# Kernel tuning notes

Hardware: AMD Instinct MI355X
Metric: run time of the kernel (lower is better)

The kernel has to match this reference:

```python
import jax, jax.numpy as jnp
import numpy as np

B, H, S, D = 2, 16, 2048, 128


def setup_inputs() -> dict:
    key = jax.random.key(0)
    kq, kk, kv, km, kb = jax.random.split(key, 5)
    q = jax.random.normal(kq, (B, H, S, D), dtype=jnp.float32)
    k = jax.random.normal(kk, (B, H, S, D), dtype=jnp.float32)
    v = jax.random.normal(kv, (B, H, S, D), dtype=jnp.float32)
    mask = jax.random.randint(km, (B, 1, S, S), 0, 2, dtype=jnp.int32)
    rel_bias = jax.random.normal(kb, (H, S, S), dtype=jnp.float32)
    return {"q": q, "k": k, "v": v, "mask": mask, "rel_bias": rel_bias}


def reference(q, k, v, mask, rel_bias):
    d_k = q.shape[-1]
    scale = 1.0 / jnp.sqrt(jnp.float32(d_k)).astype(q.dtype)
    # scores: [B,H,S,S]
    scores = jnp.einsum("bhqd,bhkd->bhqk", q, k) * scale
    scores = scores + rel_bias[None, :, :, :]  # broadcast batch
    NEG = jnp.asarray(-1e9, dtype=scores.dtype)
    scores = jnp.where(mask == 0, NEG, scores)
    attn = jax.nn.softmax(scores, axis=-1)
    # dropout p=0.0 -> identity (reference uses eval/deterministic dropout)
    out = jnp.einsum("bhqk,bhkd->bhqd", attn, v)
    return (out, attn)
```

## Files before the change

### kernel.cpp

```cpp
#include <hip/hip_runtime.h>

#define B_ 2
#define H_ 16
#define S_ 2048
#define D_ 128

typedef __attribute__((ext_vector_type(8))) short short8;
typedef __attribute__((ext_vector_type(4))) float floatx4;

__device__ __forceinline__ unsigned short f2bf(float f) {
    union { float f; unsigned int u; } c; c.f = f;
    unsigned int u = c.u;
    u += 0x7fff + ((u >> 16) & 1);
    return (unsigned short)(u >> 16);
}

__global__ __launch_bounds__(256) void vt_kernel(const float* __restrict__ v,
                                                 unsigned short* __restrict__ vt) {
    __shared__ unsigned short tl[128][66];
    int bid = blockIdx.x;
    int bh = bid >> 5;
    int s0 = (bid & 31) << 6;
    int t = threadIdx.x;
    const float4* vp = (const float4*)(v + ((size_t)bh * S_ + s0) * D_);
    #pragma unroll
    for (int i = 0; i < 8; ++i) {
        int idx = t + i * 256;
        int r = idx >> 5;
        int d = (idx & 31) << 2;
        float4 x = vp[idx];
        tl[d + 0][r] = f2bf(x.x);
        tl[d + 1][r] = f2bf(x.y);
        tl[d + 2][r] = f2bf(x.z);
        tl[d + 3][r] = f2bf(x.w);
    }
    __syncthreads();
    unsigned short* op = vt + (size_t)bh * D_ * S_ + s0;
    #pragma unroll
    for (int i = 0; i < 16; ++i) {
        int idx = t + i * 256;
        int d = idx >> 5;
        int s2 = (idx & 31) << 1;
        unsigned int val = (unsigned int)tl[d][s2] | ((unsigned int)tl[d][s2 + 1] << 16);
        *(unsigned int*)(op + (size_t)d * S_ + s2) = val;
    }
}

__global__ __launch_bounds__(256, 4) void qk_kernel(const float* __restrict__ q,
                                                    const float* __restrict__ k,
                                                    const int* __restrict__ mask,
                                                    const float* __restrict__ bias,
                                                    float* __restrict__ attn,
                                                    float* __restrict__ lsum) {
    __shared__ unsigned short q_lds[64 * 136];
    __shared__ __align__(16) char ks[17408];
    unsigned short* k_lds = (unsigned short*)ks;
    float* s_lds = (float*)ks;

    int bid = blockIdx.x;
    int qt = bid >> 5;
    int hb = bid & 31;
    int h = hb >> 1;
    int b = hb & 1;
    int bh = b * H_ + h;
    int q0 = qt << 6;
    int t = threadIdx.x;
    int w = t >> 6;
    int lane = t & 63;
    int g = lane >> 4;
    int l16 = lane & 15;
    int tr = t >> 4;
    int tc = (t & 15) << 2;

    const float4* qp = (const float4*)(q + ((size_t)bh * S_ + q0) * D_);
    #pragma unroll
    for (int i = 0; i < 8; ++i) {
        int idx = t + i * 256;
        int r = idx >> 5;
        int d = (idx & 31) << 2;
        float4 x = qp[idx];
        ushort4 y;
        y.x = f2bf(x.x); y.y = f2bf(x.y); y.z = f2bf(x.z); y.w = f2bf(x.w);
        *(ushort4*)&q_lds[r * 136 + d] = y;
    }
    __syncthreads();

    short8 afr[4];
    {
        int ro = (w * 16 + l16) * 136 + g * 8;
        #pragma unroll
        for (int kk = 0; kk < 4; ++kk)
            afr[kk] = *(const short8*)&q_lds[ro + kk * 32];
    }

    const float scale = 0.08838834764831845f;
    float rs[4] = {0.f, 0.f, 0.f, 0.f};
    const float* bias_h = bias + (size_t)h * S_ * S_;
    const int* mask_b = mask + (size_t)b * S_ * S_;
    float* attn_p = attn + (size_t)bh * S_ * S_;
    const float4* kbase = (const float4*)(k + (size_t)bh * S_ * D_);

    for (int kt = 0; kt < 32; ++kt) {
        int k0 = kt << 6;
        __syncthreads();
        const float4* kp = kbase + (size_t)k0 * (D_ / 4);
        float4 kv[8];
        #pragma unroll
        for (int i = 0; i < 8; ++i) kv[i] = kp[t + i * 256];
        float4 b4[4];
        int4 m4[4];
        #pragma unroll
        for (int i = 0; i < 4; ++i) {
            size_t off = (size_t)(q0 + tr + 16 * i) * S_ + k0 + tc;
            b4[i] = *(const float4*)&bias_h[off];
            m4[i] = *(const int4*)&mask_b[off];
        }
        #pragma unroll
        for (int i = 0; i < 8; ++i) {
            int idx = t + i * 256;
            int r = idx >> 5;
            int d = (idx & 31) << 2;
            ushort4 y;
            y.x = f2bf(kv[i].x); y.y = f2bf(kv[i].y); y.z = f2bf(kv[i].z); y.w = f2bf(kv[i].w);
            *(ushort4*)&k_lds[r * 136 + d] = y;
        }
        __syncthreads();

        floatx4 acc[4];
        #pragma unroll
        for (int nt = 0; nt < 4; ++nt) acc[nt] = (floatx4){0.f, 0.f, 0.f, 0.f};
        #pragma unroll
        for (int kk = 0; kk < 4; ++kk) {
            #pragma unroll
            for (int nt = 0; nt < 4; ++nt) {
                short8 bfr = *(const short8*)&k_lds[(nt * 16 + l16) * 136 + kk * 32 + g * 8];
                acc[nt] = __builtin_amdgcn_mfma_f32_16x16x32_bf16(afr[kk], bfr, acc[nt], 0, 0, 0);
            }
        }
        __syncthreads();

        #pragma unroll
        for (int nt = 0; nt < 4; ++nt)
            #pragma unroll
            for (int r = 0; r < 4; ++r)
                s_lds[(w * 16 + g * 4 + r) * 68 + nt * 16 + l16] = acc[nt][r];
        __syncthreads();

        #pragma unroll
        for (int i = 0; i < 4; ++i) {
            int lr = tr + 16 * i;
            float4 sv = *(const float4*)&s_lds[lr * 68 + tc];
            float4 e;
            e.x = m4[i].x ? __expf(fmaf(sv.x, scale, b4[i].x)) : 0.f;
            e.y = m4[i].y ? __expf(fmaf(sv.y, scale, b4[i].y)) : 0.f;
            e.z = m4[i].z ? __expf(fmaf(sv.z, scale, b4[i].z)) : 0.f;
            e.w = m4[i].w ? __expf(fmaf(sv.w, scale, b4[i].w)) : 0.f;
            *(float4*)&attn_p[(size_t)(q0 + lr) * S_ + k0 + tc] = e;
            rs[i] += (e.x + e.y) + (e.z + e.w);
        }
    }

    #pragma unroll
    for (int i = 0; i < 4; ++i) {
        #pragma unroll
        for (int off = 1; off < 16; off <<= 1)
            rs[i] += __shfl_xor(rs[i], off, 16);
        if ((t & 15) == 0)
            lsum[(size_t)bh * S_ + q0 + tr + 16 * i] = rs[i];
    }
}

__global__ __launch_bounds__(256, 4) void pv_kernel(float* __restrict__ attn,
                                                    const unsigned short* __restrict__ vt,
                                                    const float* __restrict__ lsum,
                                                    float* __restrict__ out) {
    __shared__ unsigned short p_lds[64 * 80];
    __shared__ unsigned short v_lds[128 * 80];
    __shared__ float rinv[64];
    int bid = blockIdx.x;
    int qt = bid >> 5;
    int hb = bid & 31;
    int h = hb >> 1;
    int b = hb & 1;
    int bh = b * H_ + h;
    int q0 = qt << 6;
    int t = threadIdx.x;
    int w = t >> 6;
    int lane = t & 63;
    int g = lane >> 4;
    int l16 = lane & 15;
    int tr = t >> 4;
    int tc = (t & 15) << 2;

    if (t < 64) {
        float lv = lsum[(size_t)bh * S_ + q0 + t];
        rinv[t] = lv > 0.f ? 1.0f / lv : 0.0f;
    }
    __syncthreads();

    floatx4 acc[8];
    #pragma unroll
    for (int nt = 0; nt < 8; ++nt) acc[nt] = (floatx4){0.f, 0.f, 0.f, 0.f};

    float* attn_p = attn + ((size_t)bh * S_ + q0) * S_;
    const unsigned short* vt_p = vt + (size_t)bh * D_ * S_;

    for (int kt = 0; kt < 32; ++kt) {
        int k0 = kt << 6;
        __syncthreads();
        #pragma unroll
        for (int i = 0; i < 4; ++i) {
            int lr = tr + 16 * i;
            float4* gp = (float4*)&attn_p[(size_t)lr * S_ + k0 + tc];
            float4 x = *gp;
            float riv = rinv[lr];
            x.x *= riv; x.y *= riv; x.z *= riv; x.w *= riv;
            *gp = x;
            ushort4 y;
            y.x = f2bf(x.x); y.y = f2bf(x.y); y.z = f2bf(x.z); y.w = f2bf(x.w);
            *(ushort4*)&p_lds[lr * 80 + tc] = y;
        }
        #pragma unroll
        for (int i = 0; i < 4; ++i) {
            int idx = t + i * 256;
            int d = idx >> 3;
            int c8 = (idx & 7) << 3;
            *(uint4*)&v_lds[d * 80 + c8] = *(const uint4*)&vt_p[(size_t)d * S_ + k0 + c8];
        }
        __syncthreads();

        #pragma unroll
        for (int kk = 0; kk < 2; ++kk) {
            short8 afr = *(const short8*)&p_lds[(w * 16 + l16) * 80 + kk * 32 + g * 8];
            #pragma unroll
            for (int nt = 0; nt < 8; ++nt) {
                short8 bfr = *(const short8*)&v_lds[(nt * 16 + l16) * 80 + kk * 32 + g * 8];
                acc[nt] = __builtin_amdgcn_mfma_f32_16x16x32_bf16(afr, bfr, acc[nt], 0, 0, 0);
            }
        }
    }

    float* op = out + ((size_t)bh * S_ + q0 + w * 16 + g * 4) * D_ + l16;
    #pragma unroll
    for (int nt = 0; nt < 8; ++nt)
        #pragma unroll
        for (int r = 0; r < 4; ++r)
            op[(size_t)r * D_ + nt * 16] = acc[nt][r];
}

extern "C" void kernel_launch(void* const* d_in, const int* in_sizes, int n_in,
                              void* d_out, int out_size, void* d_ws, size_t ws_size,
                              hipStream_t stream) {
    const float* q    = (const float*)d_in[0];
    const float* k    = (const float*)d_in[1];
    const float* v    = (const float*)d_in[2];
    const int*   mask = (const int*)d_in[3];
    const float* bias = (const float*)d_in[4];

    float* out  = (float*)d_out;
    float* attn = out + (size_t)B_ * H_ * S_ * D_;

    float* lsum = (float*)d_ws;
    unsigned short* vt = (unsigned short*)((char*)d_ws + (size_t)B_ * H_ * S_ * sizeof(float));

    int nblk = B_ * H_ * (S_ / 64);
    vt_kernel<<<nblk, 256, 0, stream>>>(v, vt);
    qk_kernel<<<nblk, 256, 0, stream>>>(q, k, mask, bias, attn, lsum);
    pv_kernel<<<nblk, 256, 0, stream>>>(attn, vt, lsum, out);
}
```

Before: 1.294 ms.

## Fuse QK and PV into two-pass attention kernel with bf16 K and async LDS loads

Replaces the separate QK and PV kernels with a single kernel. The first pass computes the row sums of exp scores. The second pass recomputes the scores, normalizes them, writes attn once and accumulates P·V directly. This avoids writing then reading back and rewriting the large fp32 attn matrix. K is pre-converted to bf16 by a new kernel and staged via global_load_lds into swizzled, double-buffered LDS, and bias/mask are prefetched into registers. The cost is recomputing QK and rereading bias/mask twice, plus higher register pressure (launch bounds lowered to 3).

Measured after the change: 1.156 ms. 10.7% less time.

```diff
diff --git a/kernel.cpp b/kernel.cpp
--- a/kernel.cpp
+++ b/kernel.cpp
@@ -13,6 +13,28 @@
     unsigned int u = c.u;
     u += 0x7fff + ((u >> 16) & 1);
     return (unsigned short)(u >> 16);
+}
+
+__device__ __forceinline__ void gld16(const void* g, void* l) {
+    __builtin_amdgcn_global_load_lds(
+        (const __attribute__((address_space(1))) unsigned int*)(unsigned long long)g,
+        (__attribute__((address_space(3))) unsigned int*)(unsigned int)(unsigned long long)l,
+        16, 0, 0);
+}
+
+__global__ __launch_bounds__(256) void kbf_kernel(const float* __restrict__ k,
+                                                  unsigned short* __restrict__ kw) {
+    int base = blockIdx.x * 1024 + threadIdx.x;
+    #pragma unroll
+    for (int i = 0; i < 4; ++i) {
+        int idx = base + i * 256;
+        const float4* s = (const float4*)k + (size_t)idx * 2;
+        float4 a = s[0], c = s[1];
+        short8 y;
+        y[0] = f2bf(a.x); y[1] = f2bf(a.y); y[2] = f2bf(a.z); y[3] = f2bf(a.w);
+        y[4] = f2bf(c.x); y[5] = f2bf(c.y); y[6] = f2bf(c.z); y[7] = f2bf(c.w);
+        ((short8*)kw)[idx] = y;
+    }
 }
 
 __global__ __launch_bounds__(256) void vt_kernel(const float* __restrict__ v,
@@ -46,16 +68,44 @@
     }
 }
 
-__global__ __launch_bounds__(256, 4) void qk_kernel(const float* __restrict__ q,
-                                                    const float* __restrict__ k,
-                                                    const int* __restrict__ mask,
-                                                    const float* __restrict__ bias,
-                                                    float* __restrict__ attn,
-                                                    float* __restrict__ lsum) {
-    __shared__ unsigned short q_lds[64 * 136];
-    __shared__ __align__(16) char ks[17408];
-    unsigned short* k_lds = (unsigned short*)ks;
-    float* s_lds = (float*)ks;
+
+#define LOAD_BM(BB, MM, K0) do {                                              \
+    _Pragma("unroll") for (int rr = 0; rr < 4; ++rr) {                        \
+        _Pragma("unroll") for (int nt = 0; nt < 4; ++nt) {                    \
+            BB[rr * 4 + nt] = bias_r[rr][(K0) + nt * 16];                     \
+            MM[rr * 4 + nt] = mask_r[rr][(K0) + nt * 16]; } } } while (0)
+
+#define QK_MFMA(KB, ACC) do {                                                 \
+    _Pragma("unroll") for (int nt = 0; nt < 4; ++nt)                          \
+        ACC[nt] = (floatx4){0.f, 0.f, 0.f, 0.f};                              \
+    _Pragma("unroll") for (int kk = 0; kk < 4; ++kk) {                        \
+        _Pragma("unroll") for (int nt = 0; nt < 4; ++nt) {                    \
+            int r_ = nt * 16 + l16;                                           \
+            short8 bfr_ = *(const short8*)((const char*)(KB) + r_ * 256 +     \
+                           ((kk * 64 + g * 16) ^ ((r_ & 7) << 4)));           \
+            ACC[nt] = __builtin_amdgcn_mfma_f32_16x16x32_bf16(                \
+                          afr[kk], bfr_, ACC[nt], 0, 0, 0); } } } while (0)
+
+#define ERS(BB, MM) do {                                                      \
+    _Pragma("unroll") for (int rr = 0; rr < 4; ++rr) {                        \
+        _Pragma("unroll") for (int nt = 0; nt < 4; ++nt) {                    \
+            float e_ = MM[rr * 4 + nt]                                        \
+                ? __expf(fmaf(acc[nt][rr], scale, BB[rr * 4 + nt])) : 0.f;    \
+            rs[rr] += e_; } } } while (0)
+
+__global__ __launch_bounds__(256, 3) void attn_kernel(
+    const float* __restrict__ q,
+    const int* __restrict__ mask,
+    const float* __restrict__ bias,
+    const unsigned short* __restrict__ ktw,
+    const unsigned short* __restrict__ vtw,
+    float* __restrict__ attn,
+    float* __restrict__ out)
+{
+    __shared__ __align__(16) char smem[40960];
+    unsigned short* kbuf0 = (unsigned short*)smem;
+    unsigned short* kbuf1 = (unsigned short*)(smem + 16384);
+    unsigned short* pbuf  = (unsigned short*)(smem + 32768);
 
     int bid = blockIdx.x;
     int qt = bid >> 5;
@@ -69,188 +119,171 @@
     int lane = t & 63;
     int g = lane >> 4;
     int l16 = lane & 15;
-    int tr = t >> 4;
-    int tc = (t & 15) << 2;
-
-    const float4* qp = (const float4*)(q + ((size_t)bh * S_ + q0) * D_);
-    #pragma unroll
-    for (int i = 0; i < 8; ++i) {
-        int idx = t + i * 256;
-        int r = idx >> 5;
-        int d = (idx & 31) << 2;
-        float4 x = qp[idx];
-        ushort4 y;
-        y.x = f2bf(x.x); y.y = f2bf(x.y); y.z = f2bf(x.z); y.w = f2bf(x.w);
-        *(ushort4*)&q_lds[r * 136 + d] = y;
-    }
-    __syncthreads();
+
+    const unsigned short* ktw_bh = ktw + (size_t)bh * S_ * D_;
+    const unsigned short* vtw_bh = vtw + (size_t)bh * D_ * S_;
 
     short8 afr[4];
     {
-        int ro = (w * 16 + l16) * 136 + g * 8;
-        #pragma unroll
-        for (int kk = 0; kk < 4; ++kk)
-            afr[kk] = *(const short8*)&q_lds[ro + kk * 32];
-    }
+        const float* qrow = q + ((size_t)bh * S_ + q0 + w * 16 + l16) * D_;
+        #pragma unroll
+        for (int kk = 0; kk < 4; ++kk) {
+            float4 a = *(const float4*)&qrow[kk * 32 + g * 8];
+            float4 c = *(const float4*)&qrow[kk * 32 + g * 8 + 4];
+            short8 f;
+            f[0] = f2bf(a.x); f[1] = f2bf(a.y); f[2] = f2bf(a.z); f[3] = f2bf(a.w);
+            f[4] = f2bf(c.x); f[5] = f2bf(c.y); f[6] = f2bf(c.z); f[7] = f2bf(c.w);
+            afr[kk] = f;
+        }
+    }
+
+    const float* bias_r[4];
+    const int*   mask_r[4];
+    {
+        const float* bh_bias = bias + (size_t)h * S_ * S_;
+        const int*   b_mask  = mask + (size_t)b * S_ * S_;
+        #pragma unroll
+        for (int rr = 0; rr < 4; ++rr) {
+            int row = q0 + w * 16 + g * 4 + rr;
+            bias_r[rr] = bh_bias + (size_t)row * S_ + l16;
+            mask_r[rr] = b_mask  + (size_t)row * S_ + l16;
+        }
+    }
+
+    auto stage_k = [&](int k0, unsigned short* kb) {
+        int rsub = lane >> 4;
+        int cb = (lane & 15) << 4;
+        #pragma unroll
+        for (int c = 0; c < 4; ++c) {
+            int r = w * 16 + c * 4 + rsub;
+            const char* src = (const char*)ktw_bh + (((size_t)(k0 + r)) << 8)
+                              + (cb ^ ((r & 7) << 4));
+            gld16(src, (char*)kb + w * 4096 + c * 1024);
+        }
+    };
+    auto stage_v = [&](int k0) {
+        int dsub = lane >> 3;
+        int cb = (lane & 7) << 4;
+        #pragma unroll
+        for (int c = 0; c < 4; ++c) {
+            int d = w * 32 + c * 8 + dsub;
+            const char* src = (const char*)vtw_bh + (size_t)d * (S_ * 2)
+                              + (size_t)(k0 * 2) + (cb ^ ((d & 7) << 4));
+            gld16(src, (char*)kbuf1 + w * 4096 + c * 1024);
+        }
+    };
 
     const float scale = 0.08838834764831845f;
     float rs[4] = {0.f, 0.f, 0.f, 0.f};
-    const float* bias_h = bias + (size_t)h * S_ * S_;
-    const int* mask_b = mask + (size_t)b * S_ * S_;
-    float* attn_p = attn + (size_t)bh * S_ * S_;
-    const float4* kbase = (const float4*)(k + (size_t)bh * S_ * D_);
-
+    float bbA[16], bbB[16];
+    int   mmA[16], mmB[16];
+
+    stage_k(0, kbuf0);
+    LOAD_BM(bbA, mmA, 0);
+    __syncthreads();
+
+    #pragma unroll 1
+    for (int ktp = 0; ktp < 16; ++ktp) {
+        int kt0 = ktp << 1;
+        stage_k((kt0 + 1) << 6, kbuf1);
+        LOAD_BM(bbB, mmB, (kt0 + 1) << 6);
+        {
+            floatx4 acc[4];
+            QK_MFMA(kbuf0, acc);
+            ERS(bbA, mmA);
+        }
+        __syncthreads();
+        if (kt0 < 30) {
+            stage_k((kt0 + 2) << 6, kbuf0);
+            LOAD_BM(bbA, mmA, (kt0 + 2) << 6);
+        }
+        {
+            floatx4 acc[4];
+            QK_MFMA(kbuf1, acc);
+            ERS(bbB, mmB);
+        }
+        __syncthreads();
+    }
+
+    float rinv[4];
+    #pragma unroll
+    for (int rr = 0; rr < 4; ++rr) {
+        float s = rs[rr];
+        s += __shfl_xor(s, 1, 16);
+        s += __shfl_xor(s, 2, 16);
+        s += __shfl_xor(s, 4, 16);
+        s += __shfl_xor(s, 8, 16);
+        rinv[rr] = s > 0.f ? 1.0f / s : 0.f;
+    }
+
+    floatx4 oacc[8];
+    #pragma unroll
+    for (int nt = 0; nt < 8; ++nt) oacc[nt] = (floatx4){0.f, 0.f, 0.f, 0.f};
+
+    stage_k(0, kbuf0);
+    stage_v(0);
+    LOAD_BM(bbA, mmA, 0);
+    __syncthreads();
+
+    float* attn_r = attn + (size_t)bh * S_ * S_
+                  + (size_t)(q0 + w * 16 + g * 4) * S_ + l16;
+
+    #pragma unroll 1
     for (int kt = 0; kt < 32; ++kt) {
         int k0 = kt << 6;
-        __syncthreads();
-        const float4* kp = kbase + (size_t)k0 * (D_ / 4);
-        float4 kv[8];
-        #pragma unroll
-        for (int i = 0; i < 8; ++i) kv[i] = kp[t + i * 256];
-        float4 b4[4];
-        int4 m4[4];
-        #pragma unroll
-        for (int i = 0; i < 4; ++i) {
-            size_t off = (size_t)(q0 + tr + 16 * i) * S_ + k0 + tc;
-            b4[i] = *(const float4*)&bias_h[off];
-            m4[i] = *(const int4*)&mask_b[off];
-        }
-        #pragma unroll
-        for (int i = 0; i < 8; ++i) {
-            int idx = t + i * 256;
-            int r = idx >> 5;
-            int d = (idx & 31) << 2;
-            ushort4 y;
-            y.x = f2bf(kv[i].x); y.y = f2bf(kv[i].y); y.z = f2bf(kv[i].z); y.w = f2bf(kv[i].w);
-            *(ushort4*)&k_lds[r * 136 + d] = y;
-        }
-        __syncthreads();
-
         floatx4 acc[4];
-        #pragma unroll
-        for (int nt = 0; nt < 4; ++nt) acc[nt] = (floatx4){0.f, 0.f, 0.f, 0.f};
-        #pragma unroll
-        for (int kk = 0; kk < 4; ++kk) {
+        QK_MFMA(kbuf0, acc);
+
+        float p[16];
+        #pragma unroll
+        for (int rr = 0; rr < 4; ++rr) {
             #pragma unroll
             for (int nt = 0; nt < 4; ++nt) {
-                short8 bfr = *(const short8*)&k_lds[(nt * 16 + l16) * 136 + kk * 32 + g * 8];
-                acc[nt] = __builtin_amdgcn_mfma_f32_16x16x32_bf16(afr[kk], bfr, acc[nt], 0, 0, 0);
+                float e_ = mmA[rr * 4 + nt]
+                    ? __expf(fmaf(acc[nt][rr], scale, bbA[rr * 4 + nt])) : 0.f;
+                float pv_ = e_ * rinv[rr];
+                p[rr * 4 + nt] = pv_;
+                int prow = g * 4 + rr;
+                *(unsigned short*)((char*)pbuf + (w << 11) + prow * 128 +
+                    ((nt * 32 + (l16 << 1)) ^ ((prow & 7) << 4))) = f2bf(pv_);
             }
         }
-        __syncthreads();
-
-        #pragma unroll
-        for (int nt = 0; nt < 4; ++nt)
-            #pragma unroll
-            for (int r = 0; r < 4; ++r)
-                s_lds[(w * 16 + g * 4 + r) * 68 + nt * 16 + l16] = acc[nt][r];
-        __syncthreads();
-
-        #pragma unroll
-        for (int i = 0; i < 4; ++i) {
-            int lr = tr + 16 * i;
-            float4 sv = *(const float4*)&s_lds[lr * 68 + tc];
-            float4 e;
-            e.x = m4[i].x ? __expf(fmaf(sv.x, scale, b4[i].x)) : 0.f;
-            e.y = m4[i].y ? __expf(fmaf(sv.y, scale, b4[i].y)) : 0.f;
-            e.z = m4[i].z ? __expf(fmaf(sv.z, scale, b4[i].z)) : 0.f;
-            e.w = m4[i].w ? __expf(fmaf(sv.w, scale, b4[i].w)) : 0.f;
-            *(float4*)&attn_p[(size_t)(q0 + lr) * S_ + k0 + tc] = e;
-            rs[i] += (e.x + e.y) + (e.z + e.w);
-        }
-    }
-
-    #pragma unroll
-    for (int i = 0; i < 4; ++i) {
-        #pragma unroll
-        for (int off = 1; off < 16; off <<= 1)
-            rs[i] += __shfl_xor(rs[i], off, 16);
-        if ((t & 15) == 0)
-            lsum[(size_t)bh * S_ + q0 + tr + 16 * i] = rs[i];
-    }
-}
-
-__global__ __launch_bounds__(256, 4) void pv_kernel(float* __restrict__ attn,
-                                                    const unsigned short* __restrict__ vt,
-                                                    const float* __restrict__ lsum,
-                                                    float* __restrict__ out) {
-    __shared__ unsigned short p_lds[64 * 80];
-    __shared__ unsigned short v_lds[128 * 80];
-    __shared__ float rinv[64];
-    int bid = blockIdx.x;
-    int qt = bid >> 5;
-    int hb = bid & 31;
-    int h = hb >> 1;
-    int b = hb & 1;
-    int bh = b * H_ + h;
-    int q0 = qt << 6;
-    int t = threadIdx.x;
-    int w = t >> 6;
-    int lane = t & 63;
-    int g = lane >> 4;
-    int l16 = lane & 15;
-    int tr = t >> 4;
-    int tc = (t & 15) << 2;
-
-    if (t < 64) {
-        float lv = lsum[(size_t)bh * S_ + q0 + t];
-        rinv[t] = lv > 0.f ? 1.0f / lv : 0.0f;
-    }
-    __syncthreads();
-
-    floatx4 acc[8];
-    #pragma unroll
-    for (int nt = 0; nt < 8; ++nt) acc[nt] = (floatx4){0.f, 0.f, 0.f, 0.f};
-
-    float* attn_p = attn + ((size_t)bh * S_ + q0) * S_;
-    const unsigned short* vt_p = vt + (size_t)bh * D_ * S_;
-
-    for (int kt = 0; kt < 32; ++kt) {
-        int k0 = kt << 6;
-        __syncthreads();
-        #pragma unroll
-        for (int i = 0; i < 4; ++i) {
-            int lr = tr + 16 * i;
-            float4* gp = (float4*)&attn_p[(size_t)lr * S_ + k0 + tc];
-            float4 x = *gp;
-            float riv = rinv[lr];
-            x.x *= riv; x.y *= riv; x.z *= riv; x.w *= riv;
-            *gp = x;
-            ushort4 y;
-            y.x = f2bf(x.x); y.y = f2bf(x.y); y.z = f2bf(x.z); y.w = f2bf(x.w);
-            *(ushort4*)&p_lds[lr * 80 + tc] = y;
-        }
-        #pragma unroll
-        for (int i = 0; i < 4; ++i) {
-            int idx = t + i * 256;
-            int d = idx >> 3;
-            int c8 = (idx & 7) << 3;
-            *(uint4*)&v_lds[d * 80 + c8] = *(const uint4*)&vt_p[(size_t)d * S_ + k0 + c8];
-        }
-        __syncthreads();
+        if (kt < 31) LOAD_BM(bbA, mmA, k0 + 64);
 
         #pragma unroll
         for (int kk = 0; kk < 2; ++kk) {
-            short8 afr = *(const short8*)&p_lds[(w * 16 + l16) * 80 + kk * 32 + g * 8];
+            short8 pa = *(const short8*)((const char*)pbuf + (w << 11) +
+                          l16 * 128 + ((kk * 64 + g * 16) ^ ((l16 & 7) << 4)));
             #pragma unroll
             for (int nt = 0; nt < 8; ++nt) {
-                short8 bfr = *(const short8*)&v_lds[(nt * 16 + l16) * 80 + kk * 32 + g * 8];
-                acc[nt] = __builtin_amdgcn_mfma_f32_16x16x32_bf16(afr, bfr, acc[nt], 0, 0, 0);
+                int d_ = nt * 16 + l16;
+                short8 vf = *(const short8*)((const char*)kbuf1 + d_ * 128 +
+                              ((kk * 64 + g * 16) ^ ((d_ & 7) << 4)));
+                oacc[nt] = __builtin_amdgcn_mfma_f32_16x16x32_bf16(pa, vf, oacc[nt], 0, 0, 0);
             }
         }
+        __syncthreads();
+        if (kt < 31) { stage_k(k0 + 64, kbuf0); stage_v(k0 + 64); }
+        #pragma unroll
+        for (int rr = 0; rr < 4; ++rr)
+            #pragma unroll
+            for (int nt = 0; nt < 4; ++nt)
+                attn_r[rr * S_ + k0 + nt * 16] = p[rr * 4 + nt];
+        __syncthreads();
     }
 
     float* op = out + ((size_t)bh * S_ + q0 + w * 16 + g * 4) * D_ + l16;
     #pragma unroll
     for (int nt = 0; nt < 8; ++nt)
         #pragma unroll
-        for (int r = 0; r < 4; ++r)
-            op[(size_t)r * D_ + nt * 16] = acc[nt][r];
+        for (int rr = 0; rr < 4; ++rr)
+            op[(size_t)rr * D_ + nt * 16] = oacc[nt][rr];
 }
 
 extern "C" void kernel_launch(void* const* d_in, const int* in_sizes, int n_in,
                               void* d_out, int out_size, void* d_ws, size_t ws_size,
                               hipStream_t stream) {
+    (void)in_sizes; (void)n_in; (void)out_size; (void)ws_size;
     const float* q    = (const float*)d_in[0];
     const float* k    = (const float*)d_in[1];
     const float* v    = (const float*)d_in[2];
@@ -260,11 +293,10 @@
     float* out  = (float*)d_out;
     float* attn = out + (size_t)B_ * H_ * S_ * D_;
 
-    float* lsum = (float*)d_ws;
-    unsigned short* vt = (unsigned short*)((char*)d_ws + (size_t)B_ * H_ * S_ * sizeof(float));
-
-    int nblk = B_ * H_ * (S_ / 64);
-    vt_kernel<<<nblk, 256, 0, stream>>>(v, vt);
-    qk_kernel<<<nblk, 256, 0, stream>>>(q, k, mask, bias, attn, lsum);
-    pv_kernel<<<nblk, 256, 0, stream>>>(attn, vt, lsum, out);
-}
+    unsigned short* ktw = (unsigned short*)d_ws;
+    unsigned short* vtw = ktw + (size_t)B_ * H_ * S_ * D_;
+
+    kbf_kernel<<<1024, 256, 0, stream>>>(k, ktw);
+    vt_kernel<<<1024, 256, 0, stream>>>(v, vtw);
+    attn_kernel<<<1024, 256, 0, stream>>>(q, mask, bias, ktw, vtw, attn, out);
+}
```
